# Optimization experiments

Measured on AMD Instinct MI355X. Metric: run time of the kernel, lower is better.

Reference implementation:

```python
import jax, jax.numpy as jnp
import numpy as np

NUM_HEADS = 8
LN_EPS = 1e-5


def _layer_norm(x, g, b):
    mu = jnp.mean(x, axis=-1, keepdims=True)
    var = jnp.mean(jnp.square(x - mu), axis=-1, keepdims=True)
    return (x - mu) * jax.lax.rsqrt(var + LN_EPS) * g + b


def setup_inputs() -> dict:
    key = jax.random.key(0)
    ks = jax.random.split(key, 8)
    B, N, D = 8, 2048, 256
    s = 0.02
    return {
        "x": jax.random.normal(ks[0], (B, N, D), jnp.float32),
        "pos": jax.random.normal(ks[1], (B, N, 2 * D), jnp.float32),
        "mask": jax.random.randint(ks[2], (B, N), 0, 2) > 0,  # True = padded key
        "Wqkv": jax.random.normal(ks[3], (D, 3 * D), jnp.float32) * s,
        "bqkv": jnp.zeros((3 * D,), jnp.float32),
        "Wpos": jax.random.normal(ks[4], (2 * D, 2 * D), jnp.float32) * s,
        "bpos": jnp.zeros((2 * D,), jnp.float32),
        "ln1_g": jnp.ones((D,), jnp.float32),
        "ln1_b": jnp.zeros((D,), jnp.float32),
        "W1": jax.random.normal(ks[5], (D, 4 * D), jnp.float32) * s,
        "b1": jnp.zeros((4 * D,), jnp.float32),
        "W2": jax.random.normal(ks[6], (4 * D, D), jnp.float32) * s,
        "b2": jnp.zeros((D,), jnp.float32),
        "ln2_g": jnp.ones((D,), jnp.float32),
        "ln2_b": jnp.zeros((D,), jnp.float32),
    }


def reference(x, pos, mask, Wqkv, bqkv, Wpos, bpos, ln1_g, ln1_b,
              W1, b1, W2, b2, ln2_g, ln2_b):
    B, N, D = x.shape
    H = NUM_HEADS
    Dh = D // H

    qkv = x @ Wqkv + bqkv                      # [B,N,3D]
    q, k, v = jnp.split(qkv, 3, axis=-1)       # each [B,N,D]
    qk_pos = pos @ Wpos + bpos                 # [B,N,2D]
    q_pos, k_pos = jnp.split(qk_pos, 2, axis=-1)
    q = q + q_pos
    k = k + k_pos

    # [B,N,D] -> [B,H,N,Dh]
    q = q.reshape(B, N, H, Dh).transpose(0, 2, 1, 3)
    k = k.reshape(B, N, H, Dh).transpose(0, 2, 1, 3)
    v = v.reshape(B, N, H, Dh).transpose(0, 2, 1, 3)

    scores = jnp.einsum('bhqd,bhkd->bhqk', q, k) / jnp.sqrt(jnp.float32(Dh))
    scores = jnp.where(mask[:, None, None, :], -jnp.inf, scores)
    attn = jax.nn.softmax(scores, axis=-1)
    out = jnp.einsum('bhqk,bhkd->bhqd', attn, v)
    out = out.transpose(0, 2, 1, 3).reshape(B, N, D)

    h = _layer_norm(x + out, ln1_g, ln1_b)
    ffn = jax.nn.relu(h @ W1 + b1) @ W2 + b2
    return _layer_norm(h + ffn, ln2_g, ln2_b)
```

## Files before the change

kernel.cpp:

```cpp
#include <hip/hip_runtime.h>
#include <math.h>

#define BATCH 8
#define SEQ   2048
#define DIM   256
#define NHEAD 8
#define DHEAD 32
#define MROWS (BATCH*SEQ)

typedef short bf16x8 __attribute__((ext_vector_type(8)));
typedef float f32x4  __attribute__((ext_vector_type(4)));

#define CLSCALE 0.25503485f

static __device__ __forceinline__ float exp2_raw(float x) {
    float r;
    asm("v_exp_f32 %0, %1" : "=v"(r) : "v"(x));
    return r;
}

static __device__ __forceinline__ unsigned bf16rne(float f) {
    unsigned u = __float_as_uint(f);
    return (u + 0x7FFFu + ((u >> 16) & 1u)) >> 16;
}

__global__ __launch_bounds__(256) void conv2_kernel(
    const float* __restrict__ s1, unsigned short* __restrict__ d1, int n1,
    const float* __restrict__ s2, unsigned short* __restrict__ d2, int n2)
{
    int i = blockIdx.x * 256 + threadIdx.x;
    const float* s; unsigned short* d; int j;
    if (i < n1) { s = s1; d = d1; j = i; }
    else { j = i - n1; if (j >= n2) return; s = s2; d = d2; }
    float4 a = ((const float4*)s)[2 * j];
    float4 b = ((const float4*)s)[2 * j + 1];
    union { unsigned short u[8]; uint4 v; } o;
    o.u[0] = bf16rne(a.x); o.u[1] = bf16rne(a.y);
    o.u[2] = bf16rne(a.z); o.u[3] = bf16rne(a.w);
    o.u[4] = bf16rne(b.x); o.u[5] = bf16rne(b.y);
    o.u[6] = bf16rne(b.z); o.u[7] = bf16rne(b.w);
    ((uint4*)d)[j] = o.v;
}

__global__ __launch_bounds__(256) void wtrans_kernel(
    const float* __restrict__ W, unsigned short* __restrict__ Wt, int K, int N)
{
    __shared__ float tile[32][33];
    const int tn0 = blockIdx.x * 32;
    const int tk0 = blockIdx.y * 32;
    const int tx = threadIdx.x & 31;
    const int ty = threadIdx.x >> 5;
    #pragma unroll
    for (int r = ty; r < 32; r += 8)
        tile[r][tx] = W[(size_t)(tk0 + r) * N + tn0 + tx];
    __syncthreads();
    #pragma unroll
    for (int r = ty; r < 32; r += 8)
        Wt[(size_t)(tn0 + r) * K + tk0 + tx] = (unsigned short)bf16rne(tile[tx][r]);
}

template<int MODE>
__global__ __launch_bounds__(256, 3) void mgemm_kernel(
    const unsigned short* __restrict__ A, const unsigned short* __restrict__ Wt,
    const float* __restrict__ bias, float* __restrict__ C,
    unsigned short* __restrict__ Cb, int M, int K, int Nc,
    const float* __restrict__ qp, const float* __restrict__ kp,
    float* __restrict__ g0, float* __restrict__ g1,
    unsigned short* __restrict__ u0, unsigned short* __restrict__ u1,
    unsigned short* __restrict__ u2)
{
    const int t    = threadIdx.x;
    const int wv   = t >> 6;
    const int lane = t & 63;
    const int g    = lane >> 4;
    const int lo   = lane & 15;
    const int wr   = wv >> 1;
    const int wc   = wv & 1;
    const int r0   = blockIdx.y * 128 + wr * 64;
    const int c0   = blockIdx.x * 128 + wc * 64;

    f32x4 acc[4][4];
    #pragma unroll
    for (int i = 0; i < 4; ++i)
        #pragma unroll
        for (int j = 0; j < 4; ++j)
            #pragma unroll
            for (int r = 0; r < 4; ++r) acc[i][j][r] = 0.f;

    const unsigned short* aP[4];
    const unsigned short* bP[4];
    #pragma unroll
    for (int i = 0; i < 4; ++i) {
        aP[i] = A  + (size_t)(r0 + 16 * i + lo) * K + g * 8;
        bP[i] = Wt + (size_t)(c0 + 16 * i + lo) * K + g * 8;
    }

    bf16x8 aA[4], bA[4], aB[4], bB[4];
    #pragma unroll
    for (int i = 0; i < 4; ++i) {
        aA[i] = *(const bf16x8*)(aP[i]);
        bA[i] = *(const bf16x8*)(bP[i]);
    }

    for (int k0 = 0; k0 < K; k0 += 64) {
        #pragma unroll
        for (int i = 0; i < 4; ++i) {
            aB[i] = *(const bf16x8*)(aP[i] + k0 + 32);
            bB[i] = *(const bf16x8*)(bP[i] + k0 + 32);
        }
        #pragma unroll
        for (int i = 0; i < 4; ++i)
            #pragma unroll
            for (int j = 0; j < 4; ++j)
                acc[i][j] = __builtin_amdgcn_mfma_f32_16x16x32_bf16(
                    aA[i], bA[j], acc[i][j], 0, 0, 0);
        if (k0 + 64 < K) {
            #pragma unroll
            for (int i = 0; i < 4; ++i) {
                aA[i] = *(const bf16x8*)(aP[i] + k0 + 64);
                bA[i] = *(const bf16x8*)(bP[i] + k0 + 64);
            }
        }
        #pragma unroll
        for (int i = 0; i < 4; ++i)
            #pragma unroll
            for (int j = 0; j < 4; ++j)
                acc[i][j] = __builtin_amdgcn_mfma_f32_16x16x32_bf16(
                    aB[i], bB[j], acc[i][j], 0, 0, 0);
    }

    #pragma unroll
    for (int j = 0; j < 4; ++j) {
        const int col = c0 + 16 * j + lo;
        const float bs = bias[col];
        #pragma unroll
        for (int i = 0; i < 4; ++i) {
            #pragma unroll
            for (int r = 0; r < 4; ++r) {
                const int row = r0 + 16 * i + g * 4 + r;
                float v = acc[i][j][r] + bs;
                if (MODE == 0) {
                    C[(size_t)row * Nc + col] = v;
                } else if (MODE == 1) {
                    Cb[(size_t)row * Nc + col] =
                        (unsigned short)bf16rne(fmaxf(v, 0.f));
                } else {
                    const int bb = row >> 11;
                    const int nn = row & (SEQ - 1);
                    const int which = col >> 8;
                    const int d  = col & 255;
                    const int hh = d >> 5;
                    const int dh = d & 31;
                    const size_t dst =
                        (((size_t)bb * NHEAD + hh) * SEQ + nn) * DHEAD + dh;
                    if (MODE == 3) {
                        (which ? g1 : g0)[dst] = v;
                    } else {
                        if (which == 2) {
                            u2[dst] = (unsigned short)bf16rne(v);
                        } else if (which == 1) {
                            v += kp[dst];
                            u1[dst] = (unsigned short)bf16rne(v);
                        } else {
                            v = (v + qp[dst]) * CLSCALE;
                            u0[dst] = (unsigned short)bf16rne(v);
                        }
                    }
                }
            }
        }
    }
}

__global__ __launch_bounds__(256) void vtrans_kernel(
    const unsigned short* __restrict__ vb, unsigned short* __restrict__ vt)
{
    int idx = blockIdx.x * 256 + threadIdx.x;
    int d   = idx & 31;
    int c   = (idx >> 5) & 255;
    int bh  = idx >> 13;
    int n0  = c * 8;
    const unsigned short* src = vb + (size_t)bh * SEQ * 32 + d;
    union { unsigned short s[8]; uint4 v; } o;
    #pragma unroll
    for (int j = 0; j < 8; ++j) o.s[j] = src[(size_t)(n0 + j) * 32];
    *(uint4*)&vt[((size_t)bh * 32 + d) * SEQ + n0] = o.v;
}

__global__ __launch_bounds__(256) void attn_kernel(
    const unsigned short* __restrict__ Qb, const unsigned short* __restrict__ Kb,
    const unsigned short* __restrict__ Vt, const int* __restrict__ mask,
    float* __restrict__ O)
{
    __shared__ float bias_s[SEQ];
    __shared__ float T[4][32][17];

    const int t    = threadIdx.x;
    const int wv   = t >> 6;
    const int lane = t & 63;
    const int g    = lane >> 4;
    const int lo   = lane & 15;

    const int sb   = ((blockIdx.x & 7) << 6) | (blockIdx.x >> 3);
    const int bh   = sb >> 3;
    const int qblk = sb & 7;
    const int bb   = bh >> 3;
    const int hh   = bh & 7;
    const int qt   = qblk * 256 + wv * 64;

    const int* mrow = mask + bb * SEQ;
    for (int i = t; i < SEQ; i += 256)
        bias_s[i] = mrow[i] ? -3.0e38f : 0.0f;
    __syncthreads();

    const unsigned short* Qh = Qb + (size_t)bh * SEQ * 32;
    const unsigned short* Kh = Kb + (size_t)bh * SEQ * 32;
    const unsigned short* Vh = Vt + (size_t)bh * 32 * SEQ;

    bf16x8 qf[4];
    #pragma unroll
    for (int i = 0; i < 4; ++i)
        qf[i] = *(const bf16x8*)&Qh[(size_t)(qt + 16 * i + lo) * 32 + g * 8];

    f32x4 acc[4][2];
    #pragma unroll
    for (int i = 0; i < 4; ++i)
        #pragma unroll
        for (int hf = 0; hf < 2; ++hf)
            #pragma unroll
            for (int r = 0; r < 4; ++r) acc[i][hf][r] = 0.f;
    float l[4] = {0.f, 0.f, 0.f, 0.f};

    const int a0 = ((((g & 1) << 5) + lo) << 2);
    const int a1 = a0 + 64;

    for (int k0 = 0; k0 < SEQ; k0 += 64) {
        bf16x8 kf[4], vf[4];
        #pragma unroll
        for (int c = 0; c < 4; ++c)
            kf[c] = *(const bf16x8*)&Kh[(size_t)(k0 + c * 16 + lo) * 32 + g * 8];
        vf[0] = *(const bf16x8*)&Vh[(size_t)lo * SEQ + k0 + g * 8];
        vf[1] = *(const bf16x8*)&Vh[(size_t)(16 + lo) * SEQ + k0 + g * 8];
        vf[2] = *(const bf16x8*)&Vh[(size_t)lo * SEQ + k0 + 32 + g * 8];
        vf[3] = *(const bf16x8*)&Vh[(size_t)(16 + lo) * SEQ + k0 + 32 + g * 8];

        f32x4 cb[4];
        #pragma unroll
        for (int c = 0; c < 4; ++c)
            cb[c] = *(const f32x4*)&bias_s[k0 + c * 16 + 4 * g];

        #pragma unroll
        for (int i = 0; i < 4; ++i) {
            f32x4 s[4];
            __builtin_amdgcn_s_setprio(1);
            #pragma unroll
            for (int c = 0; c < 4; ++c)
                s[c] = __builtin_amdgcn_mfma_f32_16x16x32_bf16(
                    kf[c], qf[i], cb[c], 0, 0, 0);
            __builtin_amdgcn_s_setprio(0);

            unsigned wA[4], wB[4];
            float tl = 0.f;
            #pragma unroll
            for (int c = 0; c < 4; ++c) {
                float p0 = exp2_raw(s[c][0]);
                float p1 = exp2_raw(s[c][1]);
                float p2 = exp2_raw(s[c][2]);
                float p3 = exp2_raw(s[c][3]);
                tl += (p0 + p1) + (p2 + p3);
                asm("v_cvt_pk_bf16_f32 %0, %1, %2"
                    : "=v"(wA[c]) : "v"(p0), "v"(p1));
                asm("v_cvt_pk_bf16_f32 %0, %1, %2"
                    : "=v"(wB[c]) : "v"(p2), "v"(p3));
            }
            l[i] += tl;

            #pragma unroll
            for (int kc = 0; kc < 2; ++kc) {
                const int c0 = 2 * kc, c1 = 2 * kc + 1;
                int x0 = __builtin_amdgcn_ds_bpermute(a0, (int)wA[c0]);
                int y0 = __builtin_amdgcn_ds_bpermute(a0, (int)wA[c1]);
                int x1 = __builtin_amdgcn_ds_bpermute(a0, (int)wB[c0]);
                int y1 = __builtin_amdgcn_ds_bpermute(a0, (int)wB[c1]);
                int x2 = __builtin_amdgcn_ds_bpermute(a1, (int)wA[c0]);
                int y2 = __builtin_amdgcn_ds_bpermute(a1, (int)wA[c1]);
                int x3 = __builtin_amdgcn_ds_bpermute(a1, (int)wB[c0]);
                int y3 = __builtin_amdgcn_ds_bpermute(a1, (int)wB[c1]);
                const bool hi2 = g >= 2;
                union { int u[4]; bf16x8 v; } pf;
                pf.u[0] = hi2 ? y0 : x0;
                pf.u[1] = hi2 ? y1 : x1;
                pf.u[2] = hi2 ? y2 : x2;
                pf.u[3] = hi2 ? y3 : x3;

                __builtin_amdgcn_s_setprio(1);
                acc[i][0] = __builtin_amdgcn_mfma_f32_16x16x32_bf16(
                    vf[2 * kc + 0], pf.v, acc[i][0], 0, 0, 0);
                acc[i][1] = __builtin_amdgcn_mfma_f32_16x16x32_bf16(
                    vf[2 * kc + 1], pf.v, acc[i][1], 0, 0, 0);
                __builtin_amdgcn_s_setprio(0);
            }
        }
    }

    #pragma unroll
    for (int i = 0; i < 4; ++i) {
        l[i] += __shfl_xor(l[i], 16);
        l[i] += __shfl_xor(l[i], 32);
        float inv = (l[i] > 0.f) ? 1.0f / l[i] : 0.f;
        #pragma unroll
        for (int hf = 0; hf < 2; ++hf)
            #pragma unroll
            for (int r = 0; r < 4; ++r)
                T[wv][hf * 16 + g * 4 + r][lo] = acc[i][hf][r] * inv;
        __syncthreads();
        #pragma unroll
        for (int p = 0; p < 2; ++p) {
            int row = p * 8 + (lane >> 3);
            int d4  = (lane & 7) * 4;
            float4 ov;
            ov.x = T[wv][d4 + 0][row];
            ov.y = T[wv][d4 + 1][row];
            ov.z = T[wv][d4 + 2][row];
            ov.w = T[wv][d4 + 3][row];
            *(float4*)&O[(size_t)(bb * SEQ + qt + i * 16 + row) * DIM + hh * 32 + d4] = ov;
        }
        __syncthreads();
    }
}

__global__ __launch_bounds__(256) void ln_kernel(
    const float* __restrict__ X, const float* __restrict__ R,
    const float* __restrict__ gam, const float* __restrict__ bet,
    float* __restrict__ Y, unsigned short* __restrict__ Yb)
{
    const int lane = threadIdx.x & 63;
    const int row  = blockIdx.x * 4 + (threadIdx.x >> 6);
    const size_t off = (size_t)row * DIM + lane * 4;

    float4 xv = *(const float4*)&X[off];
    float4 rv = *(const float4*)&R[off];
    float4 v;
    v.x = xv.x + rv.x; v.y = xv.y + rv.y;
    v.z = xv.z + rv.z; v.w = xv.w + rv.w;

    float s = (v.x + v.y) + (v.z + v.w);
    #pragma unroll
    for (int o = 1; o < 64; o <<= 1) s += __shfl_xor(s, o);
    const float mu = s * (1.f / 256.f);

    float4 d;
    d.x = v.x - mu; d.y = v.y - mu; d.z = v.z - mu; d.w = v.w - mu;
    float s2 = (d.x * d.x + d.y * d.y) + (d.z * d.z + d.w * d.w);
    #pragma unroll
    for (int o = 1; o < 64; o <<= 1) s2 += __shfl_xor(s2, o);
    const float rs = rsqrtf(s2 * (1.f / 256.f) + 1e-5f);

    float4 gv = *(const float4*)&gam[lane * 4];
    float4 bv = *(const float4*)&bet[lane * 4];
    float4 y;
    y.x = d.x * rs * gv.x + bv.x;
    y.y = d.y * rs * gv.y + bv.y;
    y.z = d.z * rs * gv.z + bv.z;
    y.w = d.w * rs * gv.w + bv.w;
    *(float4*)&Y[off] = y;

    if (Yb) {
        uint2 pk;
        pk.x = bf16rne(y.x) | (bf16rne(y.y) << 16);
        pk.y = bf16rne(y.z) | (bf16rne(y.w) << 16);
        *(uint2*)&Yb[off] = pk;
    }
}

extern "C" void kernel_launch(void* const* d_in, const int* in_sizes, int n_in,
                              void* d_out, int out_size, void* d_ws, size_t ws_size,
                              hipStream_t stream)
{
    const float* x    = (const float*)d_in[0];
    const float* pos  = (const float*)d_in[1];
    const int*   mask = (const int*)d_in[2];
    const float* Wqkv = (const float*)d_in[3];
    const float* bqkv = (const float*)d_in[4];
    const float* Wpos = (const float*)d_in[5];
    const float* bpos = (const float*)d_in[6];
    const float* ln1g = (const float*)d_in[7];
    const float* ln1b = (const float*)d_in[8];
    const float* W1   = (const float*)d_in[9];
    const float* b1   = (const float*)d_in[10];
    const float* W2   = (const float*)d_in[11];
    const float* b2   = (const float*)d_in[12];
    const float* ln2g = (const float*)d_in[13];
    const float* ln2b = (const float*)d_in[14];
    float* out = (float*)d_out;

    char* base = (char*)d_ws;
    const size_t MB = 1024 * 1024;
    const size_t SZ = (size_t)MROWS * DIM;
    float*          qp   = (float*)(base + 0);
    float*          kp   = (float*)(base + 16 * MB);
    float*          ao   = (float*)(base + 0);
    unsigned short* mid  = (unsigned short*)(base + 0);
    unsigned short* xb   = (unsigned short*)(base + 32 * MB);
    unsigned short* hb   = (unsigned short*)(base + 32 * MB);
    unsigned short* posb = (unsigned short*)(base + 40 * MB);
    float*          hbuf = (float*)(base + 40 * MB);
    unsigned short* qb   = (unsigned short*)(base + 56 * MB);
    unsigned short* kb   = (unsigned short*)(base + 64 * MB);
    unsigned short* vb   = (unsigned short*)(base + 72 * MB);
    unsigned short* vt   = (unsigned short*)(base + 80 * MB);
    unsigned short* wq   = (unsigned short*)(base + 88 * MB);
    unsigned short* wp   = wq + 768 * 256;
    unsigned short* w1   = wp + 512 * 512;
    unsigned short* w2   = w1 + 1024 * 256;
    float*          f2   = out;

    dim3 blk(256);

    conv2_kernel<<<dim3(3 * (SZ / 8) / 256), blk, 0, stream>>>(
        x, xb, SZ / 8, pos, posb, 2 * SZ / 8);
    wtrans_kernel<<<dim3(768 / 32, 256 / 32), blk, 0, stream>>>(Wqkv, wq, 256, 768);
    wtrans_kernel<<<dim3(512 / 32, 512 / 32), blk, 0, stream>>>(Wpos, wp, 512, 512);
    wtrans_kernel<<<dim3(1024 / 32, 256 / 32), blk, 0, stream>>>(W1, w1, 256, 1024);
    wtrans_kernel<<<dim3(256 / 32, 1024 / 32), blk, 0, stream>>>(W2, w2, 1024, 256);
    mgemm_kernel<3><<<dim3(512 / 128, MROWS / 128), blk, 0, stream>>>(
        posb, wp, bpos, nullptr, nullptr, MROWS, 512, 512,
        nullptr, nullptr, qp, kp, nullptr, nullptr, nullptr);
    mgemm_kernel<2><<<dim3(768 / 128, MROWS / 128), blk, 0, stream>>>(
        xb, wq, bqkv, nullptr, nullptr, MROWS, 256, 768,
        qp, kp, nullptr, nullptr, qb, kb, vb);
    vtrans_kernel<<<dim3(2048), blk, 0, stream>>>(vb, vt);
    attn_kernel<<<dim3(BATCH * NHEAD * (SEQ / 256)), blk, 0, stream>>>(
        qb, kb, vt, mask, ao);
    ln_kernel<<<dim3(MROWS / 4), blk, 0, stream>>>(x, ao, ln1g, ln1b, hbuf, hb);
    mgemm_kernel<1><<<dim3(1024 / 128, MROWS / 128), blk, 0, stream>>>(
        hb, w1, b1, nullptr, mid, MROWS, 256, 1024,
        nullptr, nullptr, nullptr, nullptr, nullptr, nullptr, nullptr);
    mgemm_kernel<0><<<dim3(256 / 128, MROWS / 128), blk, 0, stream>>>(
        mid, w2, b2, f2, nullptr, MROWS, 1024, 256,
        nullptr, nullptr, nullptr, nullptr, nullptr, nullptr, nullptr);
    ln_kernel<<<dim3(MROWS / 4), blk, 0, stream>>>(hbuf, f2, ln2g, ln2b, out, nullptr);
}
```

Measured before the change: 278.3 us.

## Fuse pos projection into QK GEMM via concatenated K dimension

The code concatenates x and pos into one bf16 activation matrix with K=768 and stacks the transposed Wqkv Q/K columns with Wpos into one weight matrix. A single GEMM then produces q+q_pos and k+k_pos directly, and a separate GEMM computes V from the x portion. This drops the fp32 qp/kp intermediate writes and reads and one full-size GEMM's epilogue traffic. In exchange, the Q/K GEMM does the same arithmetic over a longer K, and there is one extra small weight-transpose launch.

```diff
diff --git a/kernel.cpp b/kernel.cpp
--- a/kernel.cpp
+++ b/kernel.cpp
@@ -7,6 +7,7 @@
 #define NHEAD 8
 #define DHEAD 32
 #define MROWS (BATCH*SEQ)
+#define KCAT  768
 
 typedef short bf16x8 __attribute__((ext_vector_type(8)));
 typedef float f32x4  __attribute__((ext_vector_type(4)));
@@ -24,14 +25,21 @@
     return (u + 0x7FFFu + ((u >> 16) & 1u)) >> 16;
 }
 
-__global__ __launch_bounds__(256) void conv2_kernel(
-    const float* __restrict__ s1, unsigned short* __restrict__ d1, int n1,
-    const float* __restrict__ s2, unsigned short* __restrict__ d2, int n2)
+__global__ __launch_bounds__(256) void convcat_kernel(
+    const float* __restrict__ x, const float* __restrict__ pos,
+    unsigned short* __restrict__ acat, int n1, int n2)
 {
     int i = blockIdx.x * 256 + threadIdx.x;
-    const float* s; unsigned short* d; int j;
-    if (i < n1) { s = s1; d = d1; j = i; }
-    else { j = i - n1; if (j >= n2) return; s = s2; d = d2; }
+    const float* s; size_t dst; int j;
+    if (i < n1) {
+        j = i; s = x;
+        int row = j >> 5, c8 = (j & 31) * 8;
+        dst = (size_t)row * KCAT + c8;
+    } else {
+        j = i - n1; if (j >= n2) return; s = pos;
+        int row = j >> 6, c8 = (j & 63) * 8;
+        dst = (size_t)row * KCAT + 256 + c8;
+    }
     float4 a = ((const float4*)s)[2 * j];
     float4 b = ((const float4*)s)[2 * j + 1];
     union { unsigned short u[8]; uint4 v; } o;
@@ -39,11 +47,12 @@
     o.u[2] = bf16rne(a.z); o.u[3] = bf16rne(a.w);
     o.u[4] = bf16rne(b.x); o.u[5] = bf16rne(b.y);
     o.u[6] = bf16rne(b.z); o.u[7] = bf16rne(b.w);
-    ((uint4*)d)[j] = o.v;
+    *(uint4*)&acat[dst] = o.v;
 }
 
 __global__ __launch_bounds__(256) void wtrans_kernel(
-    const float* __restrict__ W, unsigned short* __restrict__ Wt, int K, int N)
+    const float* __restrict__ src, unsigned short* __restrict__ dst,
+    int srcN, int srcColOff, int dstK, int dstKOff)
 {
     __shared__ float tile[32][33];
     const int tn0 = blockIdx.x * 32;
@@ -52,20 +61,20 @@
     const int ty = threadIdx.x >> 5;
     #pragma unroll
     for (int r = ty; r < 32; r += 8)
-        tile[r][tx] = W[(size_t)(tk0 + r) * N + tn0 + tx];
+        tile[r][tx] = src[(size_t)(tk0 + r) * srcN + srcColOff + tn0 + tx];
     __syncthreads();
     #pragma unroll
     for (int r = ty; r < 32; r += 8)
-        Wt[(size_t)(tn0 + r) * K + tk0 + tx] = (unsigned short)bf16rne(tile[tx][r]);
+        dst[(size_t)(tn0 + r) * dstK + dstKOff + tk0 + tx] =
+            (unsigned short)bf16rne(tile[tx][r]);
 }
 
 template<int MODE>
 __global__ __launch_bounds__(256, 3) void mgemm_kernel(
     const unsigned short* __restrict__ A, const unsigned short* __restrict__ Wt,
-    const float* __restrict__ bias, float* __restrict__ C,
-    unsigned short* __restrict__ Cb, int M, int K, int Nc,
-    const float* __restrict__ qp, const float* __restrict__ kp,
-    float* __restrict__ g0, float* __restrict__ g1,
+    const float* __restrict__ bias, const float* __restrict__ bias2,
+    float* __restrict__ C, unsigned short* __restrict__ Cb,
+    int M, int K, int Nc, int lda,
     unsigned short* __restrict__ u0, unsigned short* __restrict__ u1,
     unsigned short* __restrict__ u2)
 {
@@ -91,7 +100,7 @@
     const unsigned short* bP[4];
     #pragma unroll
     for (int i = 0; i < 4; ++i) {
-        aP[i] = A  + (size_t)(r0 + 16 * i + lo) * K + g * 8;
+        aP[i] = A  + (size_t)(r0 + 16 * i + lo) * lda + g * 8;
         bP[i] = Wt + (size_t)(c0 + 16 * i + lo) * K + g * 8;
     }
 
@@ -132,7 +141,7 @@
     #pragma unroll
     for (int j = 0; j < 4; ++j) {
         const int col = c0 + 16 * j + lo;
-        const float bs = bias[col];
+        const float bs = bias[col] + ((MODE == 4) ? bias2[col] : 0.f);
         #pragma unroll
         for (int i = 0; i < 4; ++i) {
             #pragma unroll
@@ -144,7 +153,7 @@
                 } else if (MODE == 1) {
                     Cb[(size_t)row * Nc + col] =
                         (unsigned short)bf16rne(fmaxf(v, 0.f));
-                } else {
+                } else if (MODE == 4) {
                     const int bb = row >> 11;
                     const int nn = row & (SEQ - 1);
                     const int which = col >> 8;
@@ -153,19 +162,19 @@
                     const int dh = d & 31;
                     const size_t dst =
                         (((size_t)bb * NHEAD + hh) * SEQ + nn) * DHEAD + dh;
-                    if (MODE == 3) {
-                        (which ? g1 : g0)[dst] = v;
+                    if (which == 0) {
+                        u0[dst] = (unsigned short)bf16rne(v * CLSCALE);
                     } else {
-                        if (which == 2) {
-                            u2[dst] = (unsigned short)bf16rne(v);
-                        } else if (which == 1) {
-                            v += kp[dst];
-                            u1[dst] = (unsigned short)bf16rne(v);
-                        } else {
-                            v = (v + qp[dst]) * CLSCALE;
-                            u0[dst] = (unsigned short)bf16rne(v);
-                        }
+                        u1[dst] = (unsigned short)bf16rne(v);
                     }
+                } else {
+                    const int bb = row >> 11;
+                    const int nn = row & (SEQ - 1);
+                    const int hh = col >> 5;
+                    const int dh = col & 31;
+                    const size_t dst =
+                        (((size_t)bb * NHEAD + hh) * SEQ + nn) * DHEAD + dh;
+                    u2[dst] = (unsigned short)bf16rne(v);
                 }
             }
         }
@@ -397,47 +406,50 @@
     char* base = (char*)d_ws;
     const size_t MB = 1024 * 1024;
     const size_t SZ = (size_t)MROWS * DIM;
-    float*          qp   = (float*)(base + 0);
-    float*          kp   = (float*)(base + 16 * MB);
+    unsigned short* acat = (unsigned short*)(base + 0);
     float*          ao   = (float*)(base + 0);
     unsigned short* mid  = (unsigned short*)(base + 0);
-    unsigned short* xb   = (unsigned short*)(base + 32 * MB);
-    unsigned short* hb   = (unsigned short*)(base + 32 * MB);
-    unsigned short* posb = (unsigned short*)(base + 40 * MB);
-    float*          hbuf = (float*)(base + 40 * MB);
-    unsigned short* qb   = (unsigned short*)(base + 56 * MB);
-    unsigned short* kb   = (unsigned short*)(base + 64 * MB);
-    unsigned short* vb   = (unsigned short*)(base + 72 * MB);
-    unsigned short* vt   = (unsigned short*)(base + 80 * MB);
-    unsigned short* wq   = (unsigned short*)(base + 88 * MB);
-    unsigned short* wp   = wq + 768 * 256;
-    unsigned short* w1   = wp + 512 * 512;
+    unsigned short* qb   = (unsigned short*)(base + 34 * MB);
+    unsigned short* kb   = (unsigned short*)(base + 42 * MB);
+    unsigned short* vb   = (unsigned short*)(base + 50 * MB);
+    unsigned short* vt   = (unsigned short*)(base + 58 * MB);
+    unsigned short* hb   = (unsigned short*)(base + 66 * MB);
+    float*          hbuf = (float*)(base + 74 * MB);
+    unsigned short* wqk  = (unsigned short*)(base + 90 * MB);
+    unsigned short* wv   = wqk + 512 * 768;
+    unsigned short* w1   = wv + 256 * 256;
     unsigned short* w2   = w1 + 1024 * 256;
     float*          f2   = out;
 
     dim3 blk(256);
 
-    conv2_kernel<<<dim3(3 * (SZ / 8) / 256), blk, 0, stream>>>(
-        x, xb, SZ / 8, pos, posb, 2 * SZ / 8);
-    wtrans_kernel<<<dim3(768 / 32, 256 / 32), blk, 0, stream>>>(Wqkv, wq, 256, 768);
-    wtrans_kernel<<<dim3(512 / 32, 512 / 32), blk, 0, stream>>>(Wpos, wp, 512, 512);
-    wtrans_kernel<<<dim3(1024 / 32, 256 / 32), blk, 0, stream>>>(W1, w1, 256, 1024);
-    wtrans_kernel<<<dim3(256 / 32, 1024 / 32), blk, 0, stream>>>(W2, w2, 1024, 256);
-    mgemm_kernel<3><<<dim3(512 / 128, MROWS / 128), blk, 0, stream>>>(
-        posb, wp, bpos, nullptr, nullptr, MROWS, 512, 512,
-        nullptr, nullptr, qp, kp, nullptr, nullptr, nullptr);
-    mgemm_kernel<2><<<dim3(768 / 128, MROWS / 128), blk, 0, stream>>>(
-        xb, wq, bqkv, nullptr, nullptr, MROWS, 256, 768,
-        qp, kp, nullptr, nullptr, qb, kb, vb);
+    convcat_kernel<<<dim3((3 * (int)(SZ / 8)) / 256), blk, 0, stream>>>(
+        x, pos, acat, (int)(SZ / 8), (int)(2 * SZ / 8));
+    wtrans_kernel<<<dim3(512 / 32, 256 / 32), blk, 0, stream>>>(
+        Wqkv, wqk, 768, 0, 768, 0);
+    wtrans_kernel<<<dim3(512 / 32, 512 / 32), blk, 0, stream>>>(
+        Wpos, wqk, 512, 0, 768, 256);
+    wtrans_kernel<<<dim3(256 / 32, 256 / 32), blk, 0, stream>>>(
+        Wqkv, wv, 768, 512, 256, 0);
+    wtrans_kernel<<<dim3(1024 / 32, 256 / 32), blk, 0, stream>>>(
+        W1, w1, 1024, 0, 256, 0);
+    wtrans_kernel<<<dim3(256 / 32, 1024 / 32), blk, 0, stream>>>(
+        W2, w2, 256, 0, 1024, 0);
+    mgemm_kernel<4><<<dim3(512 / 128, MROWS / 128), blk, 0, stream>>>(
+        acat, wqk, bqkv, bpos, nullptr, nullptr, MROWS, KCAT, 512, KCAT,
+        qb, kb, nullptr);
+    mgemm_kernel<5><<<dim3(256 / 128, MROWS / 128), blk, 0, stream>>>(
+        acat, wv, bqkv + 512, nullptr, nullptr, nullptr, MROWS, 256, 256, KCAT,
+        nullptr, nullptr, vb);
     vtrans_kernel<<<dim3(2048), blk, 0, stream>>>(vb, vt);
     attn_kernel<<<dim3(BATCH * NHEAD * (SEQ / 256)), blk, 0, stream>>>(
         qb, kb, vt, mask, ao);
     ln_kernel<<<dim3(MROWS / 4), blk, 0, stream>>>(x, ao, ln1g, ln1b, hbuf, hb);
     mgemm_kernel<1><<<dim3(1024 / 128, MROWS / 128), blk, 0, stream>>>(
-        hb, w1, b1, nullptr, mid, MROWS, 256, 1024,
-        nullptr, nullptr, nullptr, nullptr, nullptr, nullptr, nullptr);
+        hb, w1, b1, nullptr, nullptr, mid, MROWS, 256, 1024, 256,
+        nullptr, nullptr, nullptr);
     mgemm_kernel<0><<<dim3(256 / 128, MROWS / 128), blk, 0, stream>>>(
-        mid, w2, b2, f2, nullptr, MROWS, 1024, 256,
-        nullptr, nullptr, nullptr, nullptr, nullptr, nullptr, nullptr);
+        mid, w2, b2, nullptr, f2, nullptr, MROWS, 1024, 256, 1024,
+        nullptr, nullptr, nullptr);
     ln_kernel<<<dim3(MROWS / 4), blk, 0, stream>>>(hbuf, f2, ln2g, ln2b, out, nullptr);
 }
```

Result: faster. 261.4 us (-6.1%).
